# Kernel optimization log

Measured on AMD Instinct MI355X. Metric: run time of the kernel, lower is better.

Reference implementation:

```python
import jax, jax.numpy as jnp
import numpy as np

NEG_SLOPE = 0.2
BN_EPS = 1e-5

def lrelu(x):
    return jnp.where(x >= 0, x, NEG_SLOPE * x)

def setup_inputs() -> dict:
    key = jax.random.key(0)
    ks = jax.random.split(key, 12)
    B, V, D = 256, 16, 512
    s = lambda fan_in: 1.0 / np.sqrt(fan_in)
    return {
        "F": jax.random.normal(ks[0], (B, V, D), dtype=jnp.float32),
        # Relation MLP: Linear(1024,512) x3 (stored as (in,out))
        "W1": jax.random.uniform(ks[1], (2 * D, D), jnp.float32, -s(2 * D), s(2 * D)),
        "b1": jax.random.uniform(ks[2], (D,), jnp.float32, -s(2 * D), s(2 * D)),
        "W2": jax.random.uniform(ks[3], (D, D), jnp.float32, -s(D), s(D)),
        "b2": jax.random.uniform(ks[4], (D,), jnp.float32, -s(D), s(D)),
        "W3": jax.random.uniform(ks[5], (D, D), jnp.float32, -s(D), s(D)),
        "b3": jax.random.uniform(ks[6], (D,), jnp.float32, -s(D), s(D)),
        # Fusion: Linear(1024,512) + BatchNorm1d(512)
        "Wf": jax.random.uniform(ks[7], (2 * D, D), jnp.float32, -s(2 * D), s(2 * D)),
        "bf": jax.random.uniform(ks[8], (D,), jnp.float32, -s(2 * D), s(2 * D)),
        "gamma": jnp.ones((D,), jnp.float32),
        "beta": jnp.zeros((D,), jnp.float32),
    }

def reference(F, W1, b1, W2, b2, W3, b3, Wf, bf, gamma, beta):
    B, V, D = F.shape
    # All-pairs broadcast + concat -> (B, V, V, 2D)
    F_i = jnp.broadcast_to(F[:, :, None, :], (B, V, V, D))
    F_j = jnp.broadcast_to(F[:, None, :, :], (B, V, V, D))
    M = jnp.concatenate([F_i, F_j], axis=-1)
    # 3-layer Relation MLP with LeakyReLU(0.2)
    h = lrelu(M @ W1 + b1)
    h = lrelu(h @ W2 + b2)
    h = lrelu(h @ W3 + b3)
    # Sum over neighbor axis (dim -2) -> (B, V, D)
    Msum = jnp.sum(h, axis=-2)
    # Fusion: concat, Linear, BatchNorm1d (training-mode batch stats), LeakyReLU
    X = jnp.concatenate([F, Msum], axis=-1).reshape(-1, 2 * D)  # (B*V, 2D)
    y = X @ Wf + bf
    mean = jnp.mean(y, axis=0)
    var = jnp.mean(jnp.square(y - mean), axis=0)  # biased var (torch BN)
    yn = (y - mean) * jax.lax.rsqrt(var + BN_EPS) * gamma + beta
    return lrelu(yn).reshape(B, V, D)
```

## Files before the change

### kernel.cpp

```cpp
#include <hip/hip_runtime.h>

using f32x4  = __attribute__((ext_vector_type(4))) float;
using bf16x8 = __attribute__((ext_vector_type(8))) __bf16;

static constexpr int DD = 512;
static constexpr int NTOK = 4096;

__device__ __forceinline__ float bf2f(unsigned short u) {
  unsigned int v = ((unsigned int)u) << 16;
  return __builtin_bit_cast(float, v);
}
__device__ __forceinline__ unsigned short f2bf(float f) {
  unsigned int u = __builtin_bit_cast(unsigned int, f);
  unsigned int r = u + 0x7fffu + ((u >> 16) & 1u);
  return (unsigned short)(r >> 16);
}
__device__ __forceinline__ float lrelu(float v) { return v >= 0.f ? v : 0.2f * v; }


__global__ __launch_bounds__(256) void k_prep(const float* __restrict__ F,
                                              const float* __restrict__ W1,
                                              const float* __restrict__ W2,
                                              const float* __restrict__ W3,
                                              const float* __restrict__ Wf,
                                              unsigned short* __restrict__ XP,
                                              unsigned short* __restrict__ W1P,
                                              unsigned short* __restrict__ W2P,
                                              unsigned short* __restrict__ W3P,
                                              unsigned short* __restrict__ WfP,
                                              float* __restrict__ sums) {
  const int bid = blockIdx.x, tid = threadIdx.x;
  if (bid < 8192) {
    int idx = (bid << 8) + tid;
    int t = idx >> 9, c = idx & 511;
    XP[((t >> 4) * 32 + (c >> 5)) * 512 + ((c >> 3) & 3) * 128 + (t & 15) * 8 + (c & 7)] = f2bf(F[idx]);
  } else if (bid < 10240) {
    int idx = ((bid - 8192) << 8) + tid;
    int k = idx >> 10, n = idx & 1023;
    float v = W1[(n < 512 ? k : 512 + k) * 512 + (n & 511)];
    W1P[((n >> 4) * 16 + (k >> 5)) * 512 + ((k >> 3) & 3) * 128 + (n & 15) * 8 + (k & 7)] = f2bf(v);
  } else if (bid < 11264) {
    int idx = ((bid - 10240) << 8) + tid;
    int k = idx >> 9, n = idx & 511;
    W2P[((n >> 4) * 16 + (k >> 5)) * 512 + ((k >> 3) & 3) * 128 + (n & 15) * 8 + (k & 7)] = f2bf(W2[idx]);
  } else if (bid < 12288) {
    int idx = ((bid - 11264) << 8) + tid;
    int k = idx >> 9, n = idx & 511;
    W3P[((n >> 4) * 16 + (k >> 5)) * 512 + ((k >> 3) & 3) * 128 + (n & 15) * 8 + (k & 7)] = f2bf(W3[idx]);
  } else if (bid < 14336) {
    int idx = ((bid - 12288) << 8) + tid;
    int k = idx >> 9, n = idx & 511;
    WfP[((n >> 4) * 32 + (k >> 5)) * 512 + ((k >> 3) & 3) * 128 + (n & 15) * 8 + (k & 7)] = f2bf(Wf[idx]);
  } else {
    reinterpret_cast<float4*>(sums)[tid] = float4{0.f, 0.f, 0.f, 0.f};
  }
}

__global__ __launch_bounds__(512) void k_gemm_ac(const unsigned short* __restrict__ XP,
                                                 const unsigned short* __restrict__ W1P,
                                                 unsigned short* __restrict__ ACP) {
  const int tid = threadIdx.x, lane = tid & 63, wid = tid >> 6;
  const int wm = wid >> 2, wn = wid & 3;
  const int l15 = lane & 15;
  const int bx = blockIdx.x, by = blockIdx.y;

  f32x4 acc[2][4];
#pragma unroll
  for (int mt = 0; mt < 2; ++mt)
#pragma unroll
    for (int nt = 0; nt < 4; ++nt) acc[mt][nt] = f32x4{0.f, 0.f, 0.f, 0.f};

  bf16x8 ca[2], cb[4], na[2], nb[4];
  auto ldA = [&](bf16x8 (&d)[2], int ks) {
#pragma unroll
    for (int mt = 0; mt < 2; ++mt)
      d[mt] = *reinterpret_cast<const bf16x8*>(XP + (((bx * 4 + wm * 2 + mt) * 32 + ks) << 9) + lane * 8);
  };
  auto ldB = [&](bf16x8 (&d)[4], int ks) {
#pragma unroll
    for (int nt = 0; nt < 4; ++nt)
      d[nt] = *reinterpret_cast<const bf16x8*>(W1P + ((((by * 16 + wn * 4 + nt) * 16) + ks) << 9) + lane * 8);
  };

  ldA(ca, 0); ldB(cb, 0);
  for (int ks = 0; ks < 16; ++ks) {
    int kn = (ks + 1) & 15;
    ldA(na, kn); ldB(nb, kn);
    __builtin_amdgcn_s_setprio(1);
#pragma unroll
    for (int mt = 0; mt < 2; ++mt)
#pragma unroll
      for (int nt = 0; nt < 4; ++nt)
        acc[mt][nt] = __builtin_amdgcn_mfma_f32_16x16x32_bf16(ca[mt], cb[nt], acc[mt][nt], 0, 0, 0);
    __builtin_amdgcn_s_setprio(0);
#pragma unroll
    for (int q = 0; q < 2; ++q) ca[q] = na[q];
#pragma unroll
    for (int q = 0; q < 4; ++q) cb[q] = nb[q];
  }
#pragma unroll
  for (int mt = 0; mt < 2; ++mt)
#pragma unroll
    for (int nt = 0; nt < 4; ++nt) {
      int col = by * 256 + wn * 64 + nt * 16 + l15;
      int panel = bx * 4 + wm * 2 + mt;
#pragma unroll
      for (int r = 0; r < 4; ++r) {
        int rowi = (lane >> 4) * 4 + r;
        ACP[(panel * 32 + (col >> 5)) * 512 + ((col >> 3) & 3) * 128 + rowi * 8 + (col & 7)] = f2bf(acc[mt][nt][r]);
      }
    }
}

__global__ __launch_bounds__(512, 2) void k_relation(const unsigned short* __restrict__ ACP,
                                                     const unsigned short* __restrict__ W2P,
                                                     const unsigned short* __restrict__ W3P,
                                                     const float* __restrict__ b1,
                                                     const float* __restrict__ b2,
                                                     const float* __restrict__ b3,
                                                     unsigned short* __restrict__ XP) {
  __shared__ unsigned short lds[65536];
  const int tid = threadIdx.x;
  const int b = blockIdx.x >> 1, half = blockIdx.x & 1;

  {
    const int r = tid >> 2;
    const int il = r >> 4, j = r & 15;
    const int rowA = half * 8 + il;
    const int c0 = (tid & 3) * 8;
#pragma unroll
    for (int cc = 0; cc < 512; cc += 32) {
      const int c = c0 + cc;
      uint4 av = *reinterpret_cast<const uint4*>(ACP + ((b * 32 + (cc >> 5)) << 9) + (c0 >> 3) * 128 + rowA * 8);
      uint4 cv = *reinterpret_cast<const uint4*>(ACP + ((b * 32 + 16 + (cc >> 5)) << 9) + (c0 >> 3) * 128 + j * 8);
      float4 bv0 = *reinterpret_cast<const float4*>(b1 + c);
      float4 bv1 = *reinterpret_cast<const float4*>(b1 + c + 4);
      unsigned int au[4] = {av.x, av.y, av.z, av.w};
      unsigned int cu[4] = {cv.x, cv.y, cv.z, cv.w};
      float bb[8] = {bv0.x, bv0.y, bv0.z, bv0.w, bv1.x, bv1.y, bv1.z, bv1.w};
      unsigned int ou[4];
#pragma unroll
      for (int q = 0; q < 4; ++q) {
        float v0 = lrelu(bf2f((unsigned short)(au[q] & 0xffffu)) +
                         bf2f((unsigned short)(cu[q] & 0xffffu)) + bb[2 * q]);
        float v1 = lrelu(bf2f((unsigned short)(au[q] >> 16)) +
                         bf2f((unsigned short)(cu[q] >> 16)) + bb[2 * q + 1]);
        ou[q] = ((unsigned int)f2bf(v1) << 16) | (unsigned int)f2bf(v0);
      }
      unsigned int byte = (unsigned int)(c * 2) ^ (unsigned int)((r & 7) << 4);
      uint4 o; o.x = ou[0]; o.y = ou[1]; o.z = ou[2]; o.w = ou[3];
      *reinterpret_cast<uint4*>(reinterpret_cast<char*>(lds) + r * 1024 + byte) = o;
    }
  }

  const int lane = tid & 63, wid = tid >> 6;
  const int l15 = lane & 15, lk = (lane >> 4) << 3;
  const unsigned int swz = (unsigned int)((l15 & 7) << 4);

  f32x4 acc[8][4];
  bf16x8 ca[4], cb[4], nb[4];

  auto ldB = [&](bf16x8 (&d)[4], const unsigned short* __restrict__ Wp, int ks) {
#pragma unroll
    for (int nt = 0; nt < 4; ++nt)
      d[nt] = *reinterpret_cast<const bf16x8*>(Wp + (((wid * 4 + nt) * 16 + ks) << 9) + lane * 8);
  };

  __syncthreads();
#pragma unroll
  for (int mt = 0; mt < 8; ++mt)
#pragma unroll
    for (int nt = 0; nt < 4; ++nt) acc[mt][nt] = f32x4{0.f, 0.f, 0.f, 0.f};
  ldB(cb, W2P, 0);
  for (int ks = 0; ks < 16; ++ks) {
    ldB(nb, W2P, (ks + 1) & 15);
    unsigned int colb = (unsigned int)((ks * 32 + lk) * 2) ^ swz;
#pragma unroll
    for (int h = 0; h < 2; ++h) {
#pragma unroll
      for (int q = 0; q < 4; ++q) {
        int row = (h * 4 + q) * 16 + l15;
        ca[q] = *reinterpret_cast<const bf16x8*>(reinterpret_cast<const char*>(lds) + row * 1024 + colb);
      }
      __builtin_amdgcn_s_setprio(1);
#pragma unroll
      for (int q = 0; q < 4; ++q)
#pragma unroll
        for (int nt = 0; nt < 4; ++nt)
          acc[h * 4 + q][nt] = __builtin_amdgcn_mfma_f32_16x16x32_bf16(ca[q], cb[nt], acc[h * 4 + q][nt], 0, 0, 0);
      __builtin_amdgcn_s_setprio(0);
    }
#pragma unroll
    for (int q = 0; q < 4; ++q) cb[q] = nb[q];
  }
  __syncthreads();
#pragma unroll
  for (int mt = 0; mt < 8; ++mt)
#pragma unroll
    for (int nt = 0; nt < 4; ++nt) {
      int col = wid * 64 + nt * 16 + l15;
      float bias = b2[col];
#pragma unroll
      for (int r = 0; r < 4; ++r) {
        int row = mt * 16 + (lane >> 4) * 4 + r;
        float v = lrelu(acc[mt][nt][r] + bias);
        unsigned int byte = (unsigned int)(col * 2) ^ (unsigned int)((row & 7) << 4);
        *reinterpret_cast<unsigned short*>(reinterpret_cast<char*>(lds) + row * 1024 + byte) = f2bf(v);
      }
    }
  __syncthreads();

#pragma unroll
  for (int mt = 0; mt < 8; ++mt)
#pragma unroll
    for (int nt = 0; nt < 4; ++nt) acc[mt][nt] = f32x4{0.f, 0.f, 0.f, 0.f};
  ldB(cb, W3P, 0);
  for (int ks = 0; ks < 16; ++ks) {
    ldB(nb, W3P, (ks + 1) & 15);
    unsigned int colb = (unsigned int)((ks * 32 + lk) * 2) ^ swz;
#pragma unroll
    for (int h = 0; h < 2; ++h) {
#pragma unroll
      for (int q = 0; q < 4; ++q) {
        int row = (h * 4 + q) * 16 + l15;
        ca[q] = *reinterpret_cast<const bf16x8*>(reinterpret_cast<const char*>(lds) + row * 1024 + colb);
      }
      __builtin_amdgcn_s_setprio(1);
#pragma unroll
      for (int q = 0; q < 4; ++q)
#pragma unroll
        for (int nt = 0; nt < 4; ++nt)
          acc[h * 4 + q][nt] = __builtin_amdgcn_mfma_f32_16x16x32_bf16(ca[q], cb[nt], acc[h * 4 + q][nt], 0, 0, 0);
      __builtin_amdgcn_s_setprio(0);
    }
#pragma unroll
    for (int q = 0; q < 4; ++q) cb[q] = nb[q];
  }
#pragma unroll
  for (int mt = 0; mt < 8; ++mt)
#pragma unroll
    for (int nt = 0; nt < 4; ++nt) {
      int col = wid * 64 + nt * 16 + l15;
      float bias = b3[col];
      float s = 0.f;
#pragma unroll
      for (int r = 0; r < 4; ++r) s += lrelu(acc[mt][nt][r] + bias);
      s += __shfl_xor(s, 16);
      s += __shfl_xor(s, 32);
      if (lane < 16) {
        XP[((b * 32 + 16 + (col >> 5)) << 9) + ((col >> 3) & 3) * 128 + (half * 8 + mt) * 8 + (col & 7)] = f2bf(s);
      }
    }
}

__global__ __launch_bounds__(512) void k_fusion(const unsigned short* __restrict__ XP,
                                                const unsigned short* __restrict__ WfP,
                                                const float* __restrict__ bfv,
                                                float* __restrict__ y,
                                                float* __restrict__ sums,
                                                float* __restrict__ sumsq) {
  const int tid = threadIdx.x, lane = tid & 63, wid = tid >> 6;
  const int wm = wid >> 2, wn = wid & 3;
  const int l15 = lane & 15;
  const int bx = blockIdx.x, by = blockIdx.y;
  const int rowbase = bx * 64 + wm * 32;
  const int colbase = by * 128 + wn * 32;

  f32x4 acc[2][2];
#pragma unroll
  for (int mt = 0; mt < 2; ++mt)
#pragma unroll
    for (int nt = 0; nt < 2; ++nt) acc[mt][nt] = f32x4{0.f, 0.f, 0.f, 0.f};

  bf16x8 ca[2], cb[2], na[2], nb[2];
  auto ldA = [&](bf16x8 (&d)[2], int ks) {
#pragma unroll
    for (int mt = 0; mt < 2; ++mt)
      d[mt] = *reinterpret_cast<const bf16x8*>(XP + (((bx * 4 + wm * 2 + mt) * 32 + ks) << 9) + lane * 8);
  };
  auto ldB = [&](bf16x8 (&d)[2], int ks) {
#pragma unroll
    for (int nt = 0; nt < 2; ++nt)
      d[nt] = *reinterpret_cast<const bf16x8*>(WfP + (((by * 8 + wn * 2 + nt) * 32 + ks) << 9) + lane * 8);
  };

  ldA(ca, 0); ldB(cb, 0);
  for (int ks = 0; ks < 32; ++ks) {
    int kn = (ks + 1) & 31;
    ldA(na, kn); ldB(nb, kn);
    __builtin_amdgcn_s_setprio(1);
#pragma unroll
    for (int mt = 0; mt < 2; ++mt)
#pragma unroll
      for (int nt = 0; nt < 2; ++nt)
        acc[mt][nt] = __builtin_amdgcn_mfma_f32_16x16x32_bf16(ca[mt], cb[nt], acc[mt][nt], 0, 0, 0);
    __builtin_amdgcn_s_setprio(0);
#pragma unroll
    for (int q = 0; q < 2; ++q) { ca[q] = na[q]; cb[q] = nb[q]; }
  }

  float s[2] = {0.f, 0.f}, q2[2] = {0.f, 0.f};
#pragma unroll
  for (int nt = 0; nt < 2; ++nt) {
    int col = colbase + nt * 16 + l15;
    float bias = bfv[col];
#pragma unroll
    for (int mt = 0; mt < 2; ++mt)
#pragma unroll
      for (int r = 0; r < 4; ++r) {
        int row = rowbase + mt * 16 + (lane >> 4) * 4 + r;
        float v = acc[mt][nt][r] + bias;
        y[row * DD + col] = v;
        s[nt] += v; q2[nt] += v * v;
      }
  }
#pragma unroll
  for (int nt = 0; nt < 2; ++nt) {
    s[nt] += __shfl_xor(s[nt], 16);  s[nt] += __shfl_xor(s[nt], 32);
    q2[nt] += __shfl_xor(q2[nt], 16); q2[nt] += __shfl_xor(q2[nt], 32);
    if (lane < 16) {
      int col = colbase + nt * 16 + l15;
      atomicAdd(&sums[col], s[nt]);
      atomicAdd(&sumsq[col], q2[nt]);
    }
  }
}

__global__ __launch_bounds__(256) void k_bnapply(const float* __restrict__ y,
                                                 const float* __restrict__ sums,
                                                 const float* __restrict__ sumsq,
                                                 const float* __restrict__ gamma,
                                                 const float* __restrict__ beta,
                                                 float* __restrict__ out) {
  int idx = blockIdx.x * 256 + threadIdx.x;
  if (idx >= NTOK * DD) return;
  int c = idx & 511;
  float mean = sums[c] * (1.0f / 4096.0f);
  float var = sumsq[c] * (1.0f / 4096.0f) - mean * mean;
  float rstd = rsqrtf(var + 1e-5f);
  float v = (y[idx] - mean) * rstd * gamma[c] + beta[c];
  out[idx] = lrelu(v);
}

extern "C" void kernel_launch(void* const* d_in, const int* in_sizes, int n_in,
                              void* d_out, int out_size, void* d_ws, size_t ws_size,
                              hipStream_t stream) {
  const float* F   = (const float*)d_in[0];
  const float* W1  = (const float*)d_in[1];
  const float* b1  = (const float*)d_in[2];
  const float* W2  = (const float*)d_in[3];
  const float* b2  = (const float*)d_in[4];
  const float* W3  = (const float*)d_in[5];
  const float* b3  = (const float*)d_in[6];
  const float* Wf  = (const float*)d_in[7];
  const float* bfv = (const float*)d_in[8];
  const float* gamma = (const float*)d_in[9];
  const float* beta  = (const float*)d_in[10];
  float* out = (float*)d_out;

  char* ws = (char*)d_ws;
  unsigned short* XP  = (unsigned short*)(ws);
  unsigned short* ACP = (unsigned short*)(ws + (8u << 20));
  unsigned short* W1P = (unsigned short*)(ws + (16u << 20));
  unsigned short* W2P = (unsigned short*)(ws + (17u << 20));
  unsigned short* W3P = (unsigned short*)(ws + (17u << 20) + (512u << 10));
  unsigned short* WfP = (unsigned short*)(ws + (18u << 20));
  float* y            = (float*)(ws + (19u << 20));
  float* sums         = (float*)(ws + (27u << 20));
  float* sumsq        = sums + 512;

  k_prep<<<14337, 256, 0, stream>>>(F, W1, W2, W3, Wf, XP, W1P, W2P, W3P, WfP, sums);
  k_gemm_ac<<<dim3(64, 4), 512, 0, stream>>>(XP, W1P, ACP);
  k_relation<<<512, 512, 0, stream>>>(ACP, W2P, W3P, b1, b2, b3, XP);
  k_fusion<<<dim3(64, 4), 512, 0, stream>>>(XP, WfP, bfv, y, sums, sumsq);
  k_bnapply<<<(NTOK * DD + 255) / 256, 256, 0, stream>>>(y, sums, sumsq, gamma, beta, out);
}
```

Measured before the change: 123.8 us.

## Transpose relation MLP GEMMs so weights stream as A and activations as B

Restructures the relation kernel so each wave loads weight fragments from global memory as the MFMA A operand and reads the activation tile from LDS as the B operand. Activations are stored in LDS in a pre-tiled fragment layout instead of a swizzled row-major layout. The per-warp output is now 128 features by 64 rows rather than 128 rows by 64 features. The neighbor-sum reduction becomes an LDS pass with coalesced vector stores instead of shuffles and scattered 2-byte global writes. The goal is fewer LDS bank conflicts and less epilogue scatter, at the cost of more global weight-fragment registers (8 per k-step) and extra barriers.

```diff
diff --git a/kernel.cpp b/kernel.cpp
--- a/kernel.cpp
+++ b/kernel.cpp
@@ -9,6 +9,12 @@
 __device__ __forceinline__ float bf2f(unsigned short u) {
   unsigned int v = ((unsigned int)u) << 16;
   return __builtin_bit_cast(float, v);
+}
+__device__ __forceinline__ float bflo(unsigned int u) {
+  return __builtin_bit_cast(float, u << 16);
+}
+__device__ __forceinline__ float bfhi(unsigned int u) {
+  return __builtin_bit_cast(float, u & 0xffff0000u);
 }
 __device__ __forceinline__ unsigned short f2bf(float f) {
   unsigned int u = __builtin_bit_cast(unsigned int, f);
@@ -127,12 +133,12 @@
     const int r = tid >> 2;
     const int il = r >> 4, j = r & 15;
     const int rowA = half * 8 + il;
-    const int c0 = (tid & 3) * 8;
-#pragma unroll
-    for (int cc = 0; cc < 512; cc += 32) {
-      const int c = c0 + cc;
-      uint4 av = *reinterpret_cast<const uint4*>(ACP + ((b * 32 + (cc >> 5)) << 9) + (c0 >> 3) * 128 + rowA * 8);
-      uint4 cv = *reinterpret_cast<const uint4*>(ACP + ((b * 32 + 16 + (cc >> 5)) << 9) + (c0 >> 3) * 128 + j * 8);
+    const int kq = tid & 3;
+#pragma unroll
+    for (int ks = 0; ks < 16; ++ks) {
+      const int c = ks * 32 + kq * 8;
+      uint4 av = *reinterpret_cast<const uint4*>(ACP + ((b * 32 + ks) << 9) + kq * 128 + rowA * 8);
+      uint4 cv = *reinterpret_cast<const uint4*>(ACP + ((b * 32 + 16 + ks) << 9) + kq * 128 + j * 8);
       float4 bv0 = *reinterpret_cast<const float4*>(b1 + c);
       float4 bv1 = *reinterpret_cast<const float4*>(b1 + c + 4);
       unsigned int au[4] = {av.x, av.y, av.z, av.w};
@@ -141,116 +147,106 @@
       unsigned int ou[4];
 #pragma unroll
       for (int q = 0; q < 4; ++q) {
-        float v0 = lrelu(bf2f((unsigned short)(au[q] & 0xffffu)) +
-                         bf2f((unsigned short)(cu[q] & 0xffffu)) + bb[2 * q]);
+        float v0 = lrelu(bflo(au[q]) + bflo(cu[q]) + bb[2 * q]);
         float v1 = lrelu(bf2f((unsigned short)(au[q] >> 16)) +
                          bf2f((unsigned short)(cu[q] >> 16)) + bb[2 * q + 1]);
         ou[q] = ((unsigned int)f2bf(v1) << 16) | (unsigned int)f2bf(v0);
       }
-      unsigned int byte = (unsigned int)(c * 2) ^ (unsigned int)((r & 7) << 4);
       uint4 o; o.x = ou[0]; o.y = ou[1]; o.z = ou[2]; o.w = ou[3];
-      *reinterpret_cast<uint4*>(reinterpret_cast<char*>(lds) + r * 1024 + byte) = o;
-    }
-  }
+      *reinterpret_cast<uint4*>(lds + (((r >> 4) * 16 + ks) << 9) + kq * 128 + (r & 15) * 8) = o;
+    }
+  }
+  __syncthreads();
 
   const int lane = tid & 63, wid = tid >> 6;
-  const int l15 = lane & 15, lk = (lane >> 4) << 3;
-  const unsigned int swz = (unsigned int)((l15 & 7) << 4);
+  const int l15 = lane & 15;
+  const int fg = wid >> 1;
+  const int rg = wid & 1;
 
   f32x4 acc[8][4];
-  bf16x8 ca[4], cb[4], nb[4];
-
-  auto ldB = [&](bf16x8 (&d)[4], const unsigned short* __restrict__ Wp, int ks) {
+  bf16x8 ca[8], na[8], cb[4];
+
+  auto ldA = [&](bf16x8 (&d)[8], const unsigned short* __restrict__ Wp, int ks) {
+#pragma unroll
+    for (int mt = 0; mt < 8; ++mt)
+      d[mt] = *reinterpret_cast<const bf16x8*>(Wp + (((fg * 8 + mt) * 16 + ks) << 9) + lane * 8);
+  };
+  auto ldB = [&](bf16x8 (&d)[4], int ks) {
 #pragma unroll
     for (int nt = 0; nt < 4; ++nt)
-      d[nt] = *reinterpret_cast<const bf16x8*>(Wp + (((wid * 4 + nt) * 16 + ks) << 9) + lane * 8);
-  };
-
-  __syncthreads();
-#pragma unroll
-  for (int mt = 0; mt < 8; ++mt)
-#pragma unroll
-    for (int nt = 0; nt < 4; ++nt) acc[mt][nt] = f32x4{0.f, 0.f, 0.f, 0.f};
-  ldB(cb, W2P, 0);
-  for (int ks = 0; ks < 16; ++ks) {
-    ldB(nb, W2P, (ks + 1) & 15);
-    unsigned int colb = (unsigned int)((ks * 32 + lk) * 2) ^ swz;
-#pragma unroll
-    for (int h = 0; h < 2; ++h) {
-#pragma unroll
-      for (int q = 0; q < 4; ++q) {
-        int row = (h * 4 + q) * 16 + l15;
-        ca[q] = *reinterpret_cast<const bf16x8*>(reinterpret_cast<const char*>(lds) + row * 1024 + colb);
+      d[nt] = *reinterpret_cast<const bf16x8*>(lds + ((((rg * 4 + nt) * 16) + ks) << 9) + lane * 8);
+  };
+  auto store_h = [&](f32x4 (&a)[8][4], const float* __restrict__ bias) {
+#pragma unroll
+    for (int mt = 0; mt < 8; ++mt) {
+      float4 bv = *reinterpret_cast<const float4*>(bias + fg * 128 + mt * 16 + (lane >> 4) * 4);
+      int ks2 = fg * 4 + (mt >> 1);
+      int kq2 = (mt & 1) * 2 + ((lane >> 4) >> 1);
+#pragma unroll
+      for (int nt = 0; nt < 4; ++nt) {
+        unsigned int w0 = f2bf(lrelu(a[mt][nt][0] + bv.x));
+        unsigned int w1 = f2bf(lrelu(a[mt][nt][1] + bv.y));
+        unsigned int w2 = f2bf(lrelu(a[mt][nt][2] + bv.z));
+        unsigned int w3 = f2bf(lrelu(a[mt][nt][3] + bv.w));
+        uint2 val; val.x = (w1 << 16) | w0; val.y = (w3 << 16) | w2;
+        int off = (((rg * 4 + nt) * 16 + ks2) << 9) + kq2 * 128 + l15 * 8 + ((lane >> 4) & 1) * 4;
+        *reinterpret_cast<uint2*>(lds + off) = val;
       }
+    }
+  };
+  auto layer = [&](const unsigned short* __restrict__ Wp) {
+#pragma unroll
+    for (int mt = 0; mt < 8; ++mt)
+#pragma unroll
+      for (int nt = 0; nt < 4; ++nt) acc[mt][nt] = f32x4{0.f, 0.f, 0.f, 0.f};
+    ldA(ca, Wp, 0);
+    for (int ks = 0; ks < 16; ++ks) {
+      ldA(na, Wp, (ks + 1) & 15);
+      ldB(cb, ks);
       __builtin_amdgcn_s_setprio(1);
 #pragma unroll
-      for (int q = 0; q < 4; ++q)
+      for (int mt = 0; mt < 8; ++mt)
 #pragma unroll
         for (int nt = 0; nt < 4; ++nt)
-          acc[h * 4 + q][nt] = __builtin_amdgcn_mfma_f32_16x16x32_bf16(ca[q], cb[nt], acc[h * 4 + q][nt], 0, 0, 0);
+          acc[mt][nt] = __builtin_amdgcn_mfma_f32_16x16x32_bf16(ca[mt], cb[nt], acc[mt][nt], 0, 0, 0);
       __builtin_amdgcn_s_setprio(0);
-    }
-#pragma unroll
-    for (int q = 0; q < 4; ++q) cb[q] = nb[q];
-  }
-  __syncthreads();
-#pragma unroll
-  for (int mt = 0; mt < 8; ++mt)
-#pragma unroll
-    for (int nt = 0; nt < 4; ++nt) {
-      int col = wid * 64 + nt * 16 + l15;
-      float bias = b2[col];
-#pragma unroll
-      for (int r = 0; r < 4; ++r) {
-        int row = mt * 16 + (lane >> 4) * 4 + r;
-        float v = lrelu(acc[mt][nt][r] + bias);
-        unsigned int byte = (unsigned int)(col * 2) ^ (unsigned int)((row & 7) << 4);
-        *reinterpret_cast<unsigned short*>(reinterpret_cast<char*>(lds) + row * 1024 + byte) = f2bf(v);
-      }
-    }
-  __syncthreads();
-
-#pragma unroll
-  for (int mt = 0; mt < 8; ++mt)
-#pragma unroll
-    for (int nt = 0; nt < 4; ++nt) acc[mt][nt] = f32x4{0.f, 0.f, 0.f, 0.f};
-  ldB(cb, W3P, 0);
-  for (int ks = 0; ks < 16; ++ks) {
-    ldB(nb, W3P, (ks + 1) & 15);
-    unsigned int colb = (unsigned int)((ks * 32 + lk) * 2) ^ swz;
-#pragma unroll
-    for (int h = 0; h < 2; ++h) {
-#pragma unroll
-      for (int q = 0; q < 4; ++q) {
-        int row = (h * 4 + q) * 16 + l15;
-        ca[q] = *reinterpret_cast<const bf16x8*>(reinterpret_cast<const char*>(lds) + row * 1024 + colb);
-      }
-      __builtin_amdgcn_s_setprio(1);
-#pragma unroll
-      for (int q = 0; q < 4; ++q)
-#pragma unroll
-        for (int nt = 0; nt < 4; ++nt)
-          acc[h * 4 + q][nt] = __builtin_amdgcn_mfma_f32_16x16x32_bf16(ca[q], cb[nt], acc[h * 4 + q][nt], 0, 0, 0);
-      __builtin_amdgcn_s_setprio(0);
-    }
-#pragma unroll
-    for (int q = 0; q < 4; ++q) cb[q] = nb[q];
-  }
-#pragma unroll
-  for (int mt = 0; mt < 8; ++mt)
-#pragma unroll
-    for (int nt = 0; nt < 4; ++nt) {
-      int col = wid * 64 + nt * 16 + l15;
-      float bias = b3[col];
-      float s = 0.f;
-#pragma unroll
-      for (int r = 0; r < 4; ++r) s += lrelu(acc[mt][nt][r] + bias);
-      s += __shfl_xor(s, 16);
-      s += __shfl_xor(s, 32);
-      if (lane < 16) {
-        XP[((b * 32 + 16 + (col >> 5)) << 9) + ((col >> 3) & 3) * 128 + (half * 8 + mt) * 8 + (col & 7)] = f2bf(s);
-      }
-    }
+#pragma unroll
+      for (int q = 0; q < 8; ++q) ca[q] = na[q];
+    }
+  };
+
+  layer(W2P);
+  __syncthreads();
+  store_h(acc, b2);
+  __syncthreads();
+
+  layer(W3P);
+  __syncthreads();
+  store_h(acc, b3);
+  __syncthreads();
+
+  {
+    const int t = wid;
+    const int fb = lane;
+    const int ks = fb >> 2, kq = fb & 3;
+    const unsigned short* base = lds + ((t * 16 + ks) << 9) + kq * 128;
+    float s[8] = {0.f, 0.f, 0.f, 0.f, 0.f, 0.f, 0.f, 0.f};
+    for (int it = 0; it < 16; ++it) {
+      int j = (it + lane) & 15;
+      uint4 v = *reinterpret_cast<const uint4*>(base + j * 8);
+      s[0] += bflo(v.x); s[1] += bfhi(v.x);
+      s[2] += bflo(v.y); s[3] += bfhi(v.y);
+      s[4] += bflo(v.z); s[5] += bfhi(v.z);
+      s[6] += bflo(v.w); s[7] += bfhi(v.w);
+    }
+    uint4 o;
+    o.x = ((unsigned int)f2bf(s[1]) << 16) | f2bf(s[0]);
+    o.y = ((unsigned int)f2bf(s[3]) << 16) | f2bf(s[2]);
+    o.z = ((unsigned int)f2bf(s[5]) << 16) | f2bf(s[4]);
+    o.w = ((unsigned int)f2bf(s[7]) << 16) | f2bf(s[6]);
+    int tg15 = half * 8 + t;
+    *reinterpret_cast<uint4*>(XP + ((b * 32 + 16 + ks) << 9) + kq * 128 + tg15 * 8) = o;
+  }
 }
 
 __global__ __launch_bounds__(512) void k_fusion(const unsigned short* __restrict__ XP,
```

Result: no change. 126.2 us (+1.9%).
